# Kernel tuning notes

Measured on AMD Instinct MI355X. Metric: run time of the kernel, lower is better.

Reference implementation:

```python
import jax, jax.numpy as jnp
import numpy as np

N = 50000      # nodes
E = 800000     # edges
F_IN = 128     # input feature dim
HID = 64       # hidden_channels
HEADS = 4      # num_heads
HD = HEADS * HID
NS = 0.2       # leaky_relu negative_slope
EPS = 1e-5     # batchnorm eps


def setup_inputs() -> dict:
    key = jax.random.key(0)
    ks = jax.random.split(key, 20)
    rn = lambda k, shp, sc=0.05: jax.random.normal(k, shp, jnp.float32) * sc
    inp = {}
    inp['x'] = jax.random.normal(ks[0], (N, F_IN), jnp.float32)
    inp['edge_index'] = jax.random.randint(ks[1], (2, E), 0, N, dtype=jnp.int32)
    inp['edge_attr'] = jax.random.uniform(ks[2], (E, 1), dtype=jnp.float32)
    # GATConv layer 0: in=F_IN, out=HID per head, concat=True
    inp['W0'] = rn(ks[3], (F_IN, HD)); inp['as0'] = rn(ks[4], (HEADS, HID)); inp['ad0'] = rn(ks[5], (HEADS, HID)); inp['b0'] = jnp.zeros((HD,), jnp.float32)
    # GATConv layer 1: in=HD, concat=True
    inp['W1'] = rn(ks[6], (HD, HD)); inp['as1'] = rn(ks[7], (HEADS, HID)); inp['ad1'] = rn(ks[8], (HEADS, HID)); inp['b1'] = jnp.zeros((HD,), jnp.float32)
    # GATConv layer 2: in=HD, concat=False (heads averaged)
    inp['W2'] = rn(ks[9], (HD, HD)); inp['as2'] = rn(ks[10], (HEADS, HID)); inp['ad2'] = rn(ks[11], (HEADS, HID)); inp['b2'] = jnp.zeros((HID,), jnp.float32)
    # BatchNorm affine params
    inp['g0'] = jnp.ones((HD,), jnp.float32); inp['be0'] = jnp.zeros((HD,), jnp.float32)
    inp['g1'] = jnp.ones((HD,), jnp.float32); inp['be1'] = jnp.zeros((HD,), jnp.float32)
    inp['g2'] = jnp.ones((HID,), jnp.float32); inp['be2'] = jnp.zeros((HID,), jnp.float32)
    # Edge MLP: (3*HID+1) -> 2*HID -> HID -> 1
    inp['Wm1'] = rn(ks[12], (3 * HID + 1, 2 * HID)); inp['bm1'] = jnp.zeros((2 * HID,), jnp.float32)
    inp['Wm2'] = rn(ks[13], (2 * HID, HID)); inp['bm2'] = jnp.zeros((HID,), jnp.float32)
    inp['Wm3'] = rn(ks[14], (HID, 1)); inp['bm3'] = jnp.zeros((1,), jnp.float32)
    return inp


def _gat(x, src, dst, W, a_s, a_d, b, concat):
    """PyG GATConv: gather -> linear -> attention -> segment softmax -> scatter-add.
    Adds self-loops (PyG default)."""
    n = x.shape[0]
    H, D = a_s.shape
    h = (x @ W).reshape(n, H, D)                       # [N, H, D]
    loop = jnp.arange(n, dtype=src.dtype)
    s = jnp.concatenate([src, loop])                   # [E+N]
    d = jnp.concatenate([dst, loop])
    alpha_src = jnp.einsum('nhd,hd->nh', h, a_s)       # [N, H]
    alpha_dst = jnp.einsum('nhd,hd->nh', h, a_d)
    e = jax.nn.leaky_relu(alpha_src[s] + alpha_dst[d], NS)   # [E+N, H]
    # numerically stable segment softmax over incoming edges per dst node
    m = jax.ops.segment_max(e, d, num_segments=n)
    ex = jnp.exp(e - m[d])
    den = jax.ops.segment_sum(ex, d, num_segments=n)
    att = ex / den[d]                                  # [E+N, H]
    out = jax.ops.segment_sum(h[s] * att[:, :, None], d, num_segments=n)  # [N, H, D]
    if concat:
        return out.reshape(n, H * D) + b
    return out.mean(axis=1) + b


def _bn(x, g, b):
    # BatchNorm1d, training-mode statistics (biased variance), deterministic
    mu = x.mean(axis=0)
    var = x.var(axis=0)
    return (x - mu) * jax.lax.rsqrt(var + EPS) * g + b


def reference(x, edge_index, edge_attr,
              W0, as0, ad0, b0, g0, be0,
              W1, as1, ad1, b1, g1, be1,
              W2, as2, ad2, b2, g2, be2,
              Wm1, bm1, Wm2, bm2, Wm3, bm3):
    src, dst = edge_index[0], edge_index[1]
    h = _gat(x, src, dst, W0, as0, ad0, b0, True)
    h = jax.nn.leaky_relu(_bn(h, g0, be0), NS)
    h = _gat(h, src, dst, W1, as1, ad1, b1, True)
    h = jax.nn.leaky_relu(_bn(h, g1, be1), NS)
    h = _gat(h, src, dst, W2, as2, ad2, b2, False)
    h = _bn(h, g2, be2)                                # [N, HID]
    hs, hd = h[src], h[dst]                            # gathers: [E, HID]
    ef = jnp.concatenate([hs, hd, jnp.abs(hs - hd), edge_attr], axis=1)  # [E, 3*HID+1]
    ef = jax.nn.leaky_relu(ef @ Wm1 + bm1, NS)
    ef = jax.nn.leaky_relu(ef @ Wm2 + bm2, NS)
    return (ef @ Wm3 + bm3).squeeze(-1)                # [E] edge logits
```

## Files before the change

### kernel.cpp

```cpp
#include <hip/hip_runtime.h>
#include <math.h>

#define Nn 50000
#define Npad 50048
#define Ee 800000
#define FIN 128
#define HIDd 64
#define NH 4
#define HD 256
#define NEG 0.2f
#define BEPS 1e-5f

typedef __attribute__((ext_vector_type(8))) short short8;
typedef __attribute__((ext_vector_type(4))) float f32x4;
typedef unsigned int uint;
typedef unsigned short ushort;

static __device__ __forceinline__ float lrelu(float x) { return x > 0.f ? x : NEG * x; }
static __device__ __forceinline__ float bf2f(ushort x) {
  return __uint_as_float(((uint)x) << 16);
}
static __device__ __forceinline__ ushort f2bf(float f) {
  uint u = __float_as_uint(f);
  return (ushort)((u + 0x7FFF + ((u >> 16) & 1)) >> 16);
}

__global__ void fill_kernel(float* __restrict__ p, float v, int n) {
  int i = blockIdx.x * 256 + threadIdx.x;
  if (i < n) p[i] = v;
}

__global__ void filli_kernel(int* __restrict__ p, int v, int n) {
  int i = blockIdx.x * 256 + threadIdx.x;
  if (i < n) p[i] = v;
}

__global__ void hist_kernel(const int* __restrict__ dst, int* __restrict__ deg) {
  int i = blockIdx.x * 256 + threadIdx.x;
  if (i < Ee) atomicAdd(&deg[dst[i]], 1);
}

__global__ __launch_bounds__(1024) void scan_kernel(const int* __restrict__ deg,
                                                    int* __restrict__ rowstart,
                                                    int* __restrict__ cursor) {
  __shared__ int ts[1024];
  const int tid = threadIdx.x;
  const int CH = (Nn + 1023) / 1024;
  const int base = tid * CH;
  int s = 0;
  for (int j = 0; j < CH; j++) {
    int idx = base + j;
    if (idx < Nn) s += deg[idx];
  }
  ts[tid] = s;
  __syncthreads();
  for (int off = 1; off < 1024; off <<= 1) {
    int v = (tid >= off) ? ts[tid - off] : 0;
    __syncthreads();
    ts[tid] += v;
    __syncthreads();
  }
  int run = (tid == 0) ? 0 : ts[tid - 1];
  for (int j = 0; j < CH; j++) {
    int idx = base + j;
    if (idx < Nn) {
      rowstart[idx] = run;
      cursor[idx] = run;
      run += deg[idx];
      if (idx == Nn - 1) rowstart[Nn] = run;
    }
  }
}

__global__ void elist_fill_kernel(const int* __restrict__ src, const int* __restrict__ dst,
                                  int* __restrict__ cursor, int* __restrict__ elist) {
  int i = blockIdx.x * 256 + threadIdx.x;
  if (i >= Ee + Nn) return;
  int s, d;
  if (i < Ee) { s = src[i]; d = dst[i]; } else { s = d = i - Ee; }
  int pos = atomicAdd(&cursor[d], 1);
  elist[pos] = s;
}

__global__ void cvt_bf16_kernel(const float* __restrict__ in, ushort* __restrict__ out, int n) {
  int i = blockIdx.x * 256 + threadIdx.x;
  if (i < n) out[i] = f2bf(in[i]);
}

__global__ void wfrag_kernel(const float* __restrict__ W, ushort* __restrict__ Wf, int K) {
  int idx = blockIdx.x * 256 + threadIdx.x;
  int total = (K >> 5) * 16 * 64 * 8;
  if (idx >= total) return;
  int j = idx & 7, lane = (idx >> 3) & 63, t = (idx >> 9) & 15, kc = idx >> 13;
  int n = t * 16 + (lane & 15);
  int k = kc * 32 + ((lane >> 4) << 3) + j;
  Wf[idx] = f2bf(W[k * 256 + n]);
}

__global__ __launch_bounds__(256) void gemm_mfma_kernel(
    const ushort* __restrict__ A, const ushort* __restrict__ Bf, ushort* __restrict__ C, int K,
    const float* __restrict__ a_s, const float* __restrict__ a_d,
    float* __restrict__ asrc, float* __restrict__ adst) {
  const int tid = threadIdx.x;
  const int w = tid >> 6, lane = tid & 63;
  const int q = lane >> 4, nn = lane & 15;
  const int m0 = blockIdx.x * 128 + w * 32;
  const int cb = blockIdx.y;
  f32x4 acc[2][8];
#pragma unroll
  for (int tm = 0; tm < 2; tm++)
#pragma unroll
    for (int t = 0; t < 8; t++) acc[tm][t] = (f32x4){0.f, 0.f, 0.f, 0.f};
  const int nkc = K >> 5;
  for (int kc = 0; kc < nkc; kc++) {
    short8 a0 = *(const short8*)(A + (size_t)(m0 + nn) * K + kc * 32 + q * 8);
    short8 a1 = *(const short8*)(A + (size_t)(m0 + 16 + nn) * K + kc * 32 + q * 8);
#pragma unroll
    for (int t = 0; t < 8; t++) {
      short8 b = *(const short8*)(Bf + ((size_t)((kc * 16 + cb * 8 + t) * 64 + lane)) * 8);
      acc[0][t] = __builtin_amdgcn_mfma_f32_16x16x32_bf16(a0, b, acc[0][t], 0, 0, 0);
      acc[1][t] = __builtin_amdgcn_mfma_f32_16x16x32_bf16(a1, b, acc[1][t], 0, 0, 0);
    }
  }
  float asv[8], adv[8];
#pragma unroll
  for (int t = 0; t < 8; t++) {
    int head = 2 * cb + (t >> 2);
    int dim = (t & 3) * 16 + nn;
    asv[t] = a_s[head * 64 + dim];
    adv[t] = a_d[head * 64 + dim];
  }
#pragma unroll
  for (int tm = 0; tm < 2; tm++) {
    float ps[2][4] = {{0.f, 0.f, 0.f, 0.f}, {0.f, 0.f, 0.f, 0.f}};
    float pd[2][4] = {{0.f, 0.f, 0.f, 0.f}, {0.f, 0.f, 0.f, 0.f}};
#pragma unroll
    for (int t = 0; t < 8; t++) {
      int hp = t >> 2;
#pragma unroll
      for (int r = 0; r < 4; r++) {
        float v = acc[tm][t][r];
        int row = m0 + tm * 16 + q * 4 + r;
        C[(size_t)row * 256 + cb * 128 + t * 16 + nn] = f2bf(v);
        ps[hp][r] = fmaf(v, asv[t], ps[hp][r]);
        pd[hp][r] = fmaf(v, adv[t], pd[hp][r]);
      }
    }
#pragma unroll
    for (int hp = 0; hp < 2; hp++)
#pragma unroll
      for (int r = 0; r < 4; r++) {
        float s = ps[hp][r], d2 = pd[hp][r];
        s += __shfl_xor(s, 1); s += __shfl_xor(s, 2);
        s += __shfl_xor(s, 4); s += __shfl_xor(s, 8);
        d2 += __shfl_xor(d2, 1); d2 += __shfl_xor(d2, 2);
        d2 += __shfl_xor(d2, 4); d2 += __shfl_xor(d2, 8);
        if (nn == 0) {
          int row = m0 + tm * 16 + q * 4 + r;
          asrc[row * 4 + 2 * cb + hp] = s;
          adst[row * 4 + 2 * cb + hp] = d2;
        }
      }
  }
}

__global__ __launch_bounds__(256) void gat_gather_kernel(
    const int* __restrict__ elist, const int* __restrict__ rowstart,
    const ushort* __restrict__ h, const float* __restrict__ asrc,
    const float* __restrict__ adst, const float* __restrict__ bias,
    ushort* __restrict__ aggb, float* __restrict__ aggf, int concat) {
  const int n = blockIdx.x * 4 + (threadIdx.x >> 6);
  const int lane = threadIdx.x & 63;
  const int hh = lane >> 4;
  const int start = rowstart[n], end = rowstart[n + 1];
  const float adstv = adst[n * 4 + hh];
  const ushort* hcol = h + lane * 4;
  float4 acc = make_float4(0.f, 0.f, 0.f, 0.f);
  float den = 0.f;
  int j = start;
  for (; j + 3 < end; j += 4) {
    int s0 = elist[j], s1 = elist[j + 1], s2 = elist[j + 2], s3 = elist[j + 3];
    float e0 = asrc[s0 * 4 + hh] + adstv;
    float e1 = asrc[s1 * 4 + hh] + adstv;
    float e2 = asrc[s2 * 4 + hh] + adstv;
    float e3 = asrc[s3 * 4 + hh] + adstv;
    ushort4 v0 = *(const ushort4*)(hcol + (size_t)s0 * HD);
    ushort4 v1 = *(const ushort4*)(hcol + (size_t)s1 * HD);
    ushort4 v2 = *(const ushort4*)(hcol + (size_t)s2 * HD);
    ushort4 v3 = *(const ushort4*)(hcol + (size_t)s3 * HD);
    float w0 = __expf(lrelu(e0)), w1 = __expf(lrelu(e1));
    float w2 = __expf(lrelu(e2)), w3 = __expf(lrelu(e3));
    den += (w0 + w1) + (w2 + w3);
    acc.x = fmaf(w0, bf2f(v0.x), acc.x); acc.y = fmaf(w0, bf2f(v0.y), acc.y);
    acc.z = fmaf(w0, bf2f(v0.z), acc.z); acc.w = fmaf(w0, bf2f(v0.w), acc.w);
    acc.x = fmaf(w1, bf2f(v1.x), acc.x); acc.y = fmaf(w1, bf2f(v1.y), acc.y);
    acc.z = fmaf(w1, bf2f(v1.z), acc.z); acc.w = fmaf(w1, bf2f(v1.w), acc.w);
    acc.x = fmaf(w2, bf2f(v2.x), acc.x); acc.y = fmaf(w2, bf2f(v2.y), acc.y);
    acc.z = fmaf(w2, bf2f(v2.z), acc.z); acc.w = fmaf(w2, bf2f(v2.w), acc.w);
    acc.x = fmaf(w3, bf2f(v3.x), acc.x); acc.y = fmaf(w3, bf2f(v3.y), acc.y);
    acc.z = fmaf(w3, bf2f(v3.z), acc.z); acc.w = fmaf(w3, bf2f(v3.w), acc.w);
  }
  for (; j < end; j++) {
    int s0 = elist[j];
    float e0 = asrc[s0 * 4 + hh] + adstv;
    ushort4 v0 = *(const ushort4*)(hcol + (size_t)s0 * HD);
    float w0 = __expf(lrelu(e0));
    den += w0;
    acc.x = fmaf(w0, bf2f(v0.x), acc.x); acc.y = fmaf(w0, bf2f(v0.y), acc.y);
    acc.z = fmaf(w0, bf2f(v0.z), acc.z); acc.w = fmaf(w0, bf2f(v0.w), acc.w);
  }
  float inv = 1.f / den;
  float o0 = acc.x * inv, o1 = acc.y * inv, o2 = acc.z * inv, o3 = acc.w * inv;
  if (concat) {
    float4 bv = *(const float4*)(bias + lane * 4);
    ushort4 ov;
    ov.x = f2bf(o0 + bv.x); ov.y = f2bf(o1 + bv.y);
    ov.z = f2bf(o2 + bv.z); ov.w = f2bf(o3 + bv.w);
    *(ushort4*)(aggb + (size_t)n * HD + lane * 4) = ov;
  } else {
    *(float4*)(aggf + (size_t)n * HD + lane * 4) = make_float4(o0, o1, o2, o3);
  }
}

__global__ void mean_heads_kernel(const float* __restrict__ agg, const float* __restrict__ b,
                                  float* __restrict__ h2) {
  int i = blockIdx.x * 256 + threadIdx.x;
  if (i >= Nn * HIDd) return;
  int n = i >> 6, dd = i & 63;
  const float* r = agg + (size_t)n * HD + dd;
  h2[i] = 0.25f * (r[0] + r[64] + r[128] + r[192]) + b[dd];
}

__global__ void bn_stats_bf16_kernel(const ushort* __restrict__ x, float* __restrict__ stats,
                                     int nrows, int C) {
  int r0 = blockIdx.x * 512;
  int tpc = 256 / C;
  int c = threadIdx.x % C;
  int ro = threadIdx.x / C;
  int rend = min(r0 + 512, nrows);
  float s = 0.f, s2 = 0.f;
  for (int r = r0 + ro; r < rend; r += tpc) {
    float v = bf2f(x[(size_t)r * C + c]);
    s += v; s2 += v * v;
  }
  atomicAdd(&stats[c], s);
  atomicAdd(&stats[C + c], s2);
}

__global__ void bn_stats_kernel(const float* __restrict__ x, float* __restrict__ stats,
                                int nrows, int C) {
  int r0 = blockIdx.x * 512;
  int tpc = 256 / C;
  int c = threadIdx.x % C;
  int ro = threadIdx.x / C;
  int rend = min(r0 + 512, nrows);
  float s = 0.f, s2 = 0.f;
  for (int r = r0 + ro; r < rend; r += tpc) {
    float v = x[(size_t)r * C + c];
    s += v; s2 += v * v;
  }
  atomicAdd(&stats[c], s);
  atomicAdd(&stats[C + c], s2);
}

__global__ void bn_apply_inplace_kernel(ushort* __restrict__ x, const float* __restrict__ stats,
                                        const float* __restrict__ g, const float* __restrict__ be,
                                        int C) {
  int i = blockIdx.x * 256 + threadIdx.x;
  if (i >= Nn * C) return;
  int c = i % C;
  float mu = stats[c] * (1.f / Nn);
  float var = stats[C + c] * (1.f / Nn) - mu * mu;
  float y = (bf2f(x[i]) - mu) * rsqrtf(var + BEPS) * g[c] + be[c];
  x[i] = f2bf(lrelu(y));
}

__global__ void bn_apply_bf16_kernel(const float* __restrict__ x, const float* __restrict__ stats,
                                     const float* __restrict__ g, const float* __restrict__ be,
                                     ushort* __restrict__ outb, int C) {
  int i = blockIdx.x * 256 + threadIdx.x;
  if (i >= Nn * C) return;
  int c = i % C;
  float mu = stats[c] * (1.f / Nn);
  float var = stats[C + c] * (1.f / Nn) - mu * mu;
  float y = (x[i] - mu) * rsqrtf(var + BEPS) * g[c] + be[c];
  outb[i] = f2bf(y);
}

__global__ void w1frag_kernel(const float* __restrict__ Wm1, ushort* __restrict__ W1f) {
  int idx = blockIdx.x * 256 + threadIdx.x;
  if (idx >= 7 * 8 * 64 * 8) return;
  int j = idx & 7, lane = (idx >> 3) & 63, tile = (idx >> 9) & 7, chunk = idx >> 12;
  int n = tile * 16 + (lane & 15);
  int k = chunk * 32 + (lane >> 4) * 8 + j;
  W1f[idx] = (k < 193) ? f2bf(Wm1[k * 128 + n]) : (ushort)0;
}

__global__ void w2frag_kernel(const float* __restrict__ Wm2, ushort* __restrict__ W2f) {
  int idx = blockIdx.x * 256 + threadIdx.x;
  if (idx >= 4 * 4 * 64 * 8) return;
  int j = idx & 7, lane = (idx >> 3) & 63, tile = (idx >> 9) & 3, chunk = idx >> 11;
  int n = tile * 16 + (lane & 15);
  int k = chunk * 32 + (lane >> 4) * 8 + j;
  W2f[idx] = f2bf(Wm2[k * 64 + n]);
}

static __device__ __forceinline__ short8 absdiff8(short8 a, short8 b) {
  short8 r;
#pragma unroll
  for (int j = 0; j < 8; j++) r[j] = (short)f2bf(fabsf(bf2f((ushort)a[j]) - bf2f((ushort)b[j])));
  return r;
}

#define MLP1_STEP(c, e0x, e1x)                                                         \
  {                                                                                    \
    short8 _a0 = (e0x);                                                                \
    short8 _a1 = (e1x);                                                                \
    const uint4* bp = (const uint4*)W1f + (c) * 512 + lane;                            \
    _Pragma("unroll") for (int t = 0; t < 8; t++) {                                    \
      uint4 braw = bp[t * 64];                                                         \
      short8 b = *(short8*)&braw;                                                      \
      acc0[t] = __builtin_amdgcn_mfma_f32_16x16x32_bf16(_a0, b, acc0[t], 0, 0, 0);     \
      acc1[t] = __builtin_amdgcn_mfma_f32_16x16x32_bf16(_a1, b, acc1[t], 0, 0, 0);     \
    }                                                                                  \
  }

__global__ __launch_bounds__(256) void edge_mlp_mfma_kernel(
    const ushort* __restrict__ hb, const int* __restrict__ src, const int* __restrict__ dst,
    const float* __restrict__ eattr, const ushort* __restrict__ W1f,
    const ushort* __restrict__ W2f, const float* __restrict__ bm1,
    const float* __restrict__ bm2, const float* __restrict__ Wm3,
    const float* __restrict__ bm3, float* __restrict__ out) {
  __shared__ ushort t1s[4][16 * 136];
  const int tid = threadIdx.x;
  const int w = tid >> 6, lane = tid & 63;
  const int q = lane >> 4, nn = lane & 15;

  float bm1v[8];
#pragma unroll
  for (int t = 0; t < 8; t++) bm1v[t] = bm1[t * 16 + nn];
  float bm2v[4], w3v[4];
#pragma unroll
  for (int t = 0; t < 4; t++) { bm2v[t] = bm2[t * 16 + nn]; w3v[t] = Wm3[t * 16 + nn]; }
  const float bm3v = bm3[0];

  const int base = blockIdx.x * 128 + w * 32;
  const int e0 = base + nn, e1 = base + 16 + nn;
  const int s0 = src[e0], d0 = dst[e0];
  const int s1 = src[e1], d1 = dst[e1];
  const float at0 = eattr[e0], at1 = eattr[e1];

  short8 hs0a = *(const short8*)(hb + s0 * 64 + q * 8);
  short8 hs0b = *(const short8*)(hb + s0 * 64 + 32 + q * 8);
  short8 hd0a = *(const short8*)(hb + d0 * 64 + q * 8);
  short8 hd0b = *(const short8*)(hb + d0 * 64 + 32 + q * 8);
  short8 hs1a = *(const short8*)(hb + s1 * 64 + q * 8);
  short8 hs1b = *(const short8*)(hb + s1 * 64 + 32 + q * 8);
  short8 hd1a = *(const short8*)(hb + d1 * 64 + q * 8);
  short8 hd1b = *(const short8*)(hb + d1 * 64 + 32 + q * 8);

  f32x4 acc0[8], acc1[8];
#pragma unroll
  for (int t = 0; t < 8; t++) {
    acc0[t] = (f32x4){0.f, 0.f, 0.f, 0.f};
    acc1[t] = (f32x4){0.f, 0.f, 0.f, 0.f};
  }

  short8 a6_0 = 0, a6_1 = 0;
  if (q == 0) { a6_0[0] = (short)f2bf(at0); a6_1[0] = (short)f2bf(at1); }

  MLP1_STEP(0, hs0a, hs1a)
  MLP1_STEP(1, hs0b, hs1b)
  MLP1_STEP(2, hd0a, hd1a)
  MLP1_STEP(3, hd0b, hd1b)
  MLP1_STEP(4, absdiff8(hs0a, hd0a), absdiff8(hs1a, hd1a))
  MLP1_STEP(5, absdiff8(hs0b, hd0b), absdiff8(hs1b, hd1b))
  MLP1_STEP(6, a6_0, a6_1)

  ushort* myt1 = t1s[w];
  auto do_group = [&](f32x4* acc, int g) {
#pragma unroll
    for (int t = 0; t < 8; t++)
#pragma unroll
      for (int r = 0; r < 4; r++)
        myt1[(q * 4 + r) * 136 + t * 16 + nn] = f2bf(lrelu(acc[t][r] + bm1v[t]));
    f32x4 acc2[4];
#pragma unroll
    for (int t = 0; t < 4; t++) acc2[t] = (f32x4){0.f, 0.f, 0.f, 0.f};
#pragma unroll
    for (int c2 = 0; c2 < 4; c2++) {
      short8 a = *(short8*)&myt1[nn * 136 + c2 * 32 + q * 8];
#pragma unroll
      for (int t = 0; t < 4; t++) {
        short8 b = *(const short8*)(W2f + ((size_t)(c2 * 4 + t) * 64 + lane) * 8);
        acc2[t] = __builtin_amdgcn_mfma_f32_16x16x32_bf16(a, b, acc2[t], 0, 0, 0);
      }
    }
#pragma unroll
    for (int r = 0; r < 4; r++) {
      float sum = 0.f;
#pragma unroll
      for (int t = 0; t < 4; t++) sum += lrelu(acc2[t][r] + bm2v[t]) * w3v[t];
      sum += __shfl_xor(sum, 1);
      sum += __shfl_xor(sum, 2);
      sum += __shfl_xor(sum, 4);
      sum += __shfl_xor(sum, 8);
      if (nn == 0) out[base + g * 16 + q * 4 + r] = sum + bm3v;
    }
  };
  do_group(acc0, 0);
  do_group(acc1, 1);
}

extern "C" void kernel_launch(void* const* d_in, const int* in_sizes, int n_in,
                              void* d_out, int out_size, void* d_ws, size_t ws_size,
                              hipStream_t stream) {
  const float* x    = (const float*)d_in[0];
  const int*   ei   = (const int*)d_in[1];
  const float* eatt = (const float*)d_in[2];
  const float* W0 = (const float*)d_in[3];
  const float* as0 = (const float*)d_in[4];
  const float* ad0 = (const float*)d_in[5];
  const float* b0 = (const float*)d_in[6];
  const float* W1 = (const float*)d_in[7];
  const float* as1 = (const float*)d_in[8];
  const float* ad1 = (const float*)d_in[9];
  const float* b1 = (const float*)d_in[10];
  const float* W2 = (const float*)d_in[11];
  const float* as2 = (const float*)d_in[12];
  const float* ad2 = (const float*)d_in[13];
  const float* b2 = (const float*)d_in[14];
  const float* g0 = (const float*)d_in[15];
  const float* be0 = (const float*)d_in[16];
  const float* g1 = (const float*)d_in[17];
  const float* be1 = (const float*)d_in[18];
  const float* g2 = (const float*)d_in[19];
  const float* be2 = (const float*)d_in[20];
  const float* Wm1 = (const float*)d_in[21];
  const float* bm1 = (const float*)d_in[22];
  const float* Wm2 = (const float*)d_in[23];
  const float* bm2 = (const float*)d_in[24];
  const float* Wm3 = (const float*)d_in[25];
  const float* bm3 = (const float*)d_in[26];
  const int* src = ei;
  const int* dst = ei + Ee;
  float* out = (float*)d_out;

  char* w = (char*)d_ws;
  float*  agg  = (float*)w;
  ushort* xb   = (ushort*)w;
  ushort* hB   = (ushort*)(w + (size_t)Npad * 256 * 4);
  float*  h2   = (float*)hB;
  ushort* aggb = (ushort*)(w + (size_t)Npad * 256 * 6);
  ushort* hb2  = aggb;
  float*  asrc = (float*)(w + (size_t)Npad * 256 * 8);
  float*  adst = asrc + (size_t)Npad * 4;
  float*  stats = adst + (size_t)Npad * 4;
  int* deg      = (int*)(stats + 512);
  int* rowstart = deg + Nn;
  int* cursor   = rowstart + Nn + 16;
  int* elist    = cursor + Nn;
  ushort* W0f  = (ushort*)(elist + Ee + Nn);
  ushort* W1gf = W0f + 32768;
  ushort* W2gf = W1gf + 65536;
  ushort* eW1f = W2gf + 65536;
  ushort* eW2f = eW1f + 28672;

  filli_kernel<<<(Nn + 255) / 256, 256, 0, stream>>>(deg, 1, Nn);
  hist_kernel<<<(Ee + 255) / 256, 256, 0, stream>>>(dst, deg);
  scan_kernel<<<1, 1024, 0, stream>>>(deg, rowstart, cursor);
  elist_fill_kernel<<<(Ee + Nn + 255) / 256, 256, 0, stream>>>(src, dst, cursor, elist);

  wfrag_kernel<<<(32768 + 255) / 256, 256, 0, stream>>>(W0, W0f, FIN);
  wfrag_kernel<<<(65536 + 255) / 256, 256, 0, stream>>>(W1, W1gf, HD);
  wfrag_kernel<<<(65536 + 255) / 256, 256, 0, stream>>>(W2, W2gf, HD);
  w1frag_kernel<<<(7 * 8 * 64 * 8 + 255) / 256, 256, 0, stream>>>(Wm1, eW1f);
  w2frag_kernel<<<(4 * 4 * 64 * 8 + 255) / 256, 256, 0, stream>>>(Wm2, eW2f);

  auto gat = [&](const ushort* Ab, const ushort* Wf, int K, const float* a_s,
                 const float* a_d, const float* bias, bool concat) {
    gemm_mfma_kernel<<<dim3(Npad / 128, 2), 256, 0, stream>>>(Ab, Wf, hB, K, a_s, a_d,
                                                              asrc, adst);
    gat_gather_kernel<<<Nn / 4, 256, 0, stream>>>(elist, rowstart, hB, asrc, adst, bias,
                                                  aggb, agg, concat ? 1 : 0);
  };

  cvt_bf16_kernel<<<(Nn * FIN + 255) / 256, 256, 0, stream>>>(x, xb, Nn * FIN);
  gat(xb, W0f, FIN, as0, ad0, b0, true);
  fill_kernel<<<2, 256, 0, stream>>>(stats, 0.f, 512);
  bn_stats_bf16_kernel<<<(Nn + 511) / 512, 256, 0, stream>>>(aggb, stats, Nn, HD);
  bn_apply_inplace_kernel<<<(Nn * HD + 255) / 256, 256, 0, stream>>>(aggb, stats, g0, be0, HD);
  gat(aggb, W1gf, HD, as1, ad1, b1, true);
  fill_kernel<<<2, 256, 0, stream>>>(stats, 0.f, 512);
  bn_stats_bf16_kernel<<<(Nn + 511) / 512, 256, 0, stream>>>(aggb, stats, Nn, HD);
  bn_apply_inplace_kernel<<<(Nn * HD + 255) / 256, 256, 0, stream>>>(aggb, stats, g1, be1, HD);
  gat(aggb, W2gf, HD, as2, ad2, b2, false);
  mean_heads_kernel<<<(Nn * HIDd + 255) / 256, 256, 0, stream>>>(agg, b2, h2);
  fill_kernel<<<1, 256, 0, stream>>>(stats, 0.f, 128);
  bn_stats_kernel<<<(Nn + 511) / 512, 256, 0, stream>>>(h2, stats, Nn, HIDd);
  bn_apply_bf16_kernel<<<(Nn * HIDd + 255) / 256, 256, 0, stream>>>(h2, stats, g2, be2, hb2,
                                                                    HIDd);
  edge_mlp_mfma_kernel<<<Ee / 128, 256, 0, stream>>>(hb2, src, dst, eatt, eW1f, eW2f, bm1, bm2,
                                                     Wm3, bm3, out);
}
```

Before: 1.144 ms.

## Precompute fp16 attention weights, unroll gather by 8, fuse head-mean into gather

A new kernel computes exp(leaky_relu(asrc+adst)) once per edge and head and stores it as fp16 in an edge-ordered list. The gather kernel then reads these weights contiguously instead of doing a dependent random asrc lookup and exp per lane, and it unrolls to 8 edges so more row loads are in flight. The head-mean for the last layer is done with cross-lane shuffles inside the gather, which removes the separate mean_heads kernel and its fp32 intermediate write. The edge MLP reorders its neighbour loads to reduce register pressure. In exchange there is an extra kernel launch and extra weight-list traffic, and fp16 weights lose some precision.

Result: slower. 1.219 ms (+6.6%).

```diff
diff --git a/kernel.cpp b/kernel.cpp
--- a/kernel.cpp
+++ b/kernel.cpp
@@ -1,4 +1,5 @@
 #include <hip/hip_runtime.h>
+#include <hip/hip_fp16.h>
 #include <math.h>
 
 #define Nn 50000
@@ -164,50 +165,63 @@
   }
 }
 
+__global__ __launch_bounds__(256) void wexp_kernel(
+    const int* __restrict__ elist, const int* __restrict__ rowstart,
+    const float* __restrict__ asrc, const float* __restrict__ adst,
+    __half* __restrict__ wlist) {
+  const int n = blockIdx.x * 4 + (threadIdx.x >> 6);
+  const int lane = threadIdx.x & 63;
+  const int slot = lane >> 2, hh = lane & 3;
+  const int start = rowstart[n], end = rowstart[n + 1];
+  const float adstv = adst[n * 4 + hh];
+  for (int j = start + slot; j < end; j += 16) {
+    int s = elist[j];
+    wlist[(size_t)j * 4 + hh] = __float2half(__expf(lrelu(asrc[s * 4 + hh] + adstv)));
+  }
+}
+
 __global__ __launch_bounds__(256) void gat_gather_kernel(
     const int* __restrict__ elist, const int* __restrict__ rowstart,
-    const ushort* __restrict__ h, const float* __restrict__ asrc,
-    const float* __restrict__ adst, const float* __restrict__ bias,
-    ushort* __restrict__ aggb, float* __restrict__ aggf, int concat) {
+    const ushort* __restrict__ h, const __half* __restrict__ wlist,
+    const float* __restrict__ bias, ushort* __restrict__ aggb,
+    float* __restrict__ h2, int concat) {
   const int n = blockIdx.x * 4 + (threadIdx.x >> 6);
   const int lane = threadIdx.x & 63;
   const int hh = lane >> 4;
   const int start = rowstart[n], end = rowstart[n + 1];
-  const float adstv = adst[n * 4 + hh];
   const ushort* hcol = h + lane * 4;
+  const __half* wl = wlist + hh;
   float4 acc = make_float4(0.f, 0.f, 0.f, 0.f);
   float den = 0.f;
   int j = start;
-  for (; j + 3 < end; j += 4) {
-    int s0 = elist[j], s1 = elist[j + 1], s2 = elist[j + 2], s3 = elist[j + 3];
-    float e0 = asrc[s0 * 4 + hh] + adstv;
-    float e1 = asrc[s1 * 4 + hh] + adstv;
-    float e2 = asrc[s2 * 4 + hh] + adstv;
-    float e3 = asrc[s3 * 4 + hh] + adstv;
-    ushort4 v0 = *(const ushort4*)(hcol + (size_t)s0 * HD);
-    ushort4 v1 = *(const ushort4*)(hcol + (size_t)s1 * HD);
-    ushort4 v2 = *(const ushort4*)(hcol + (size_t)s2 * HD);
-    ushort4 v3 = *(const ushort4*)(hcol + (size_t)s3 * HD);
-    float w0 = __expf(lrelu(e0)), w1 = __expf(lrelu(e1));
-    float w2 = __expf(lrelu(e2)), w3 = __expf(lrelu(e3));
-    den += (w0 + w1) + (w2 + w3);
-    acc.x = fmaf(w0, bf2f(v0.x), acc.x); acc.y = fmaf(w0, bf2f(v0.y), acc.y);
-    acc.z = fmaf(w0, bf2f(v0.z), acc.z); acc.w = fmaf(w0, bf2f(v0.w), acc.w);
-    acc.x = fmaf(w1, bf2f(v1.x), acc.x); acc.y = fmaf(w1, bf2f(v1.y), acc.y);
-    acc.z = fmaf(w1, bf2f(v1.z), acc.z); acc.w = fmaf(w1, bf2f(v1.w), acc.w);
-    acc.x = fmaf(w2, bf2f(v2.x), acc.x); acc.y = fmaf(w2, bf2f(v2.y), acc.y);
-    acc.z = fmaf(w2, bf2f(v2.z), acc.z); acc.w = fmaf(w2, bf2f(v2.w), acc.w);
-    acc.x = fmaf(w3, bf2f(v3.x), acc.x); acc.y = fmaf(w3, bf2f(v3.y), acc.y);
-    acc.z = fmaf(w3, bf2f(v3.z), acc.z); acc.w = fmaf(w3, bf2f(v3.w), acc.w);
+  for (; j + 7 < end; j += 8) {
+    int ss[8];
+    float ww[8];
+    ushort4 vv[8];
+#pragma unroll
+    for (int k = 0; k < 8; k++) ss[k] = elist[j + k];
+#pragma unroll
+    for (int k = 0; k < 8; k++) ww[k] = __half2float(wl[(size_t)(j + k) * 4]);
+#pragma unroll
+    for (int k = 0; k < 8; k++) vv[k] = *(const ushort4*)(hcol + (size_t)ss[k] * HD);
+#pragma unroll
+    for (int k = 0; k < 8; k++) {
+      den += ww[k];
+      acc.x = fmaf(ww[k], bf2f(vv[k].x), acc.x);
+      acc.y = fmaf(ww[k], bf2f(vv[k].y), acc.y);
+      acc.z = fmaf(ww[k], bf2f(vv[k].z), acc.z);
+      acc.w = fmaf(ww[k], bf2f(vv[k].w), acc.w);
+    }
   }
   for (; j < end; j++) {
     int s0 = elist[j];
-    float e0 = asrc[s0 * 4 + hh] + adstv;
+    float w0 = __half2float(wl[(size_t)j * 4]);
     ushort4 v0 = *(const ushort4*)(hcol + (size_t)s0 * HD);
-    float w0 = __expf(lrelu(e0));
     den += w0;
-    acc.x = fmaf(w0, bf2f(v0.x), acc.x); acc.y = fmaf(w0, bf2f(v0.y), acc.y);
-    acc.z = fmaf(w0, bf2f(v0.z), acc.z); acc.w = fmaf(w0, bf2f(v0.w), acc.w);
+    acc.x = fmaf(w0, bf2f(v0.x), acc.x);
+    acc.y = fmaf(w0, bf2f(v0.y), acc.y);
+    acc.z = fmaf(w0, bf2f(v0.z), acc.z);
+    acc.w = fmaf(w0, bf2f(v0.w), acc.w);
   }
   float inv = 1.f / den;
   float o0 = acc.x * inv, o1 = acc.y * inv, o2 = acc.z * inv, o3 = acc.w * inv;
@@ -218,17 +232,17 @@
     ov.z = f2bf(o2 + bv.z); ov.w = f2bf(o3 + bv.w);
     *(ushort4*)(aggb + (size_t)n * HD + lane * 4) = ov;
   } else {
-    *(float4*)(aggf + (size_t)n * HD + lane * 4) = make_float4(o0, o1, o2, o3);
-  }
-}
-
-__global__ void mean_heads_kernel(const float* __restrict__ agg, const float* __restrict__ b,
-                                  float* __restrict__ h2) {
-  int i = blockIdx.x * 256 + threadIdx.x;
-  if (i >= Nn * HIDd) return;
-  int n = i >> 6, dd = i & 63;
-  const float* r = agg + (size_t)n * HD + dd;
-  h2[i] = 0.25f * (r[0] + r[64] + r[128] + r[192]) + b[dd];
+    o0 += __shfl_xor(o0, 16); o0 += __shfl_xor(o0, 32);
+    o1 += __shfl_xor(o1, 16); o1 += __shfl_xor(o1, 32);
+    o2 += __shfl_xor(o2, 16); o2 += __shfl_xor(o2, 32);
+    o3 += __shfl_xor(o3, 16); o3 += __shfl_xor(o3, 32);
+    if (lane < 16) {
+      float4 bv = *(const float4*)(bias + lane * 4);
+      *(float4*)(h2 + (size_t)n * 64 + lane * 4) =
+          make_float4(o0 * 0.25f + bv.x, o1 * 0.25f + bv.y,
+                      o2 * 0.25f + bv.z, o3 * 0.25f + bv.w);
+    }
+  }
 }
 
 __global__ void bn_stats_bf16_kernel(const ushort* __restrict__ x, float* __restrict__ stats,
@@ -336,28 +350,10 @@
   const int w = tid >> 6, lane = tid & 63;
   const int q = lane >> 4, nn = lane & 15;
 
-  float bm1v[8];
-#pragma unroll
-  for (int t = 0; t < 8; t++) bm1v[t] = bm1[t * 16 + nn];
-  float bm2v[4], w3v[4];
-#pragma unroll
-  for (int t = 0; t < 4; t++) { bm2v[t] = bm2[t * 16 + nn]; w3v[t] = Wm3[t * 16 + nn]; }
-  const float bm3v = bm3[0];
-
   const int base = blockIdx.x * 128 + w * 32;
   const int e0 = base + nn, e1 = base + 16 + nn;
   const int s0 = src[e0], d0 = dst[e0];
   const int s1 = src[e1], d1 = dst[e1];
-  const float at0 = eattr[e0], at1 = eattr[e1];
-
-  short8 hs0a = *(const short8*)(hb + s0 * 64 + q * 8);
-  short8 hs0b = *(const short8*)(hb + s0 * 64 + 32 + q * 8);
-  short8 hd0a = *(const short8*)(hb + d0 * 64 + q * 8);
-  short8 hd0b = *(const short8*)(hb + d0 * 64 + 32 + q * 8);
-  short8 hs1a = *(const short8*)(hb + s1 * 64 + q * 8);
-  short8 hs1b = *(const short8*)(hb + s1 * 64 + 32 + q * 8);
-  short8 hd1a = *(const short8*)(hb + d1 * 64 + q * 8);
-  short8 hd1b = *(const short8*)(hb + d1 * 64 + 32 + q * 8);
 
   f32x4 acc0[8], acc1[8];
 #pragma unroll
@@ -366,16 +362,40 @@
     acc1[t] = (f32x4){0.f, 0.f, 0.f, 0.f};
   }
 
-  short8 a6_0 = 0, a6_1 = 0;
-  if (q == 0) { a6_0[0] = (short)f2bf(at0); a6_1[0] = (short)f2bf(at1); }
-
-  MLP1_STEP(0, hs0a, hs1a)
-  MLP1_STEP(1, hs0b, hs1b)
-  MLP1_STEP(2, hd0a, hd1a)
-  MLP1_STEP(3, hd0b, hd1b)
-  MLP1_STEP(4, absdiff8(hs0a, hd0a), absdiff8(hs1a, hd1a))
-  MLP1_STEP(5, absdiff8(hs0b, hd0b), absdiff8(hs1b, hd1b))
-  MLP1_STEP(6, a6_0, a6_1)
+  {
+    short8 hs0a = *(const short8*)(hb + s0 * 64 + q * 8);
+    short8 hd0a = *(const short8*)(hb + d0 * 64 + q * 8);
+    short8 hs1a = *(const short8*)(hb + s1 * 64 + q * 8);
+    short8 hd1a = *(const short8*)(hb + d1 * 64 + q * 8);
+    MLP1_STEP(0, hs0a, hs1a)
+    MLP1_STEP(2, hd0a, hd1a)
+    MLP1_STEP(4, absdiff8(hs0a, hd0a), absdiff8(hs1a, hd1a))
+  }
+  {
+    short8 hs0b = *(const short8*)(hb + s0 * 64 + 32 + q * 8);
+    short8 hd0b = *(const short8*)(hb + d0 * 64 + 32 + q * 8);
+    short8 hs1b = *(const short8*)(hb + s1 * 64 + 32 + q * 8);
+    short8 hd1b = *(const short8*)(hb + d1 * 64 + 32 + q * 8);
+    MLP1_STEP(1, hs0b, hs1b)
+    MLP1_STEP(3, hd0b, hd1b)
+    MLP1_STEP(5, absdiff8(hs0b, hd0b), absdiff8(hs1b, hd1b))
+  }
+  {
+    short8 a6_0 = 0, a6_1 = 0;
+    if (q == 0) {
+      a6_0[0] = (short)f2bf(eattr[e0]);
+      a6_1[0] = (short)f2bf(eattr[e1]);
+    }
+    MLP1_STEP(6, a6_0, a6_1)
+  }
+
+  float bm1v[8];
+#pragma unroll
+  for (int t = 0; t < 8; t++) bm1v[t] = bm1[t * 16 + nn];
+  float bm2v[4], w3v[4];
+#pragma unroll
+  for (int t = 0; t < 4; t++) { bm2v[t] = bm2[t * 16 + nn]; w3v[t] = Wm3[t * 16 + nn]; }
+  const float bm3v = bm3[0];
 
   ushort* myt1 = t1s[w];
   auto do_group = [&](f32x4* acc, int g) {
@@ -447,12 +467,12 @@
   float* out = (float*)d_out;
 
   char* w = (char*)d_ws;
-  float*  agg  = (float*)w;
-  ushort* xb   = (ushort*)w;
+  ushort* xb    = (ushort*)w;
+  __half* wlist = (__half*)w;
   ushort* hB   = (ushort*)(w + (size_t)Npad * 256 * 4);
-  float*  h2   = (float*)hB;
   ushort* aggb = (ushort*)(w + (size_t)Npad * 256 * 6);
-  ushort* hb2  = aggb;
+  float*  h2   = (float*)aggb;
+  ushort* hb2  = (ushort*)(w + (size_t)Npad * 256 * 6 + (size_t)Nn * 64 * 4);
   float*  asrc = (float*)(w + (size_t)Npad * 256 * 8);
   float*  adst = asrc + (size_t)Npad * 4;
   float*  stats = adst + (size_t)Npad * 4;
@@ -481,8 +501,9 @@
                  const float* a_d, const float* bias, bool concat) {
     gemm_mfma_kernel<<<dim3(Npad / 128, 2), 256, 0, stream>>>(Ab, Wf, hB, K, a_s, a_d,
                                                               asrc, adst);
-    gat_gather_kernel<<<Nn / 4, 256, 0, stream>>>(elist, rowstart, hB, asrc, adst, bias,
-                                                  aggb, agg, concat ? 1 : 0);
+    wexp_kernel<<<Nn / 4, 256, 0, stream>>>(elist, rowstart, asrc, adst, wlist);
+    gat_gather_kernel<<<Nn / 4, 256, 0, stream>>>(elist, rowstart, hB, wlist, bias,
+                                                  aggb, h2, concat ? 1 : 0);
   };
 
   cvt_bf16_kernel<<<(Nn * FIN + 255) / 256, 256, 0, stream>>>(x, xb, Nn * FIN);
@@ -495,7 +516,6 @@
   bn_stats_bf16_kernel<<<(Nn + 511) / 512, 256, 0, stream>>>(aggb, stats, Nn, HD);
   bn_apply_inplace_kernel<<<(Nn * HD + 255) / 256, 256, 0, stream>>>(aggb, stats, g1, be1, HD);
   gat(aggb, W2gf, HD, as2, ad2, b2, false);
-  mean_heads_kernel<<<(Nn * HIDd + 255) / 256, 256, 0, stream>>>(agg, b2, h2);
   fill_kernel<<<1, 256, 0, stream>>>(stats, 0.f, 128);
   bn_stats_kernel<<<(Nn + 511) / 512, 256, 0, stream>>>(h2, stats, Nn, HIDd);
   bn_apply_bf16_kernel<<<(Nn * HIDd + 255) / 256, 256, 0, stream>>>(h2, stats, g2, be2, hb2,
```
